# Kernel tuning notes

Hardware: AMD Instinct MI355X
Metric: run time of the kernel (lower is better)

## Reference

```python
import jax, jax.numpy as jnp
import numpy as np

N, D_IN, D_C, D_Q, K = 4096, 64, 32, 128, 3


def setup_inputs() -> dict:
    key = jax.random.key(0)
    ks = jax.random.split(key, 16)
    rn = lambda k, shp, s: jax.random.normal(k, shp, dtype=jnp.float32) * s
    inp = {
        "x": rn(ks[0], (N, D_IN), 1.0),
        "comms": rn(ks[1], (N, D_C), 0.1),
        # dense positive transition matrix (all entries nonzero -> the
        # trans==0 -> -inf masking step is a faithful no-op here)
        "trans": jax.random.uniform(ks[2], (N, N), dtype=jnp.float32, minval=0.01, maxval=1.0),
        "mask": jnp.ones((N,), dtype=jnp.int32),
        # encoding: Linear(num_inputs + comm_channels, ch_q)
        "W_enc": rn(ks[3], (D_IN + D_C, D_Q), 1.0 / np.sqrt(D_IN + D_C)),
        "b_enc": rn(ks[4], (D_Q,), 0.01),
        # att_decoding[k]: Linear(ch_q, ch_q)
        "W_ad": rn(ks[5], (K, D_Q, D_Q), 1.0 / np.sqrt(D_Q)),
        "b_ad": rn(ks[6], (K, D_Q), 0.01),
        # att[k]: Linear(2*ch_q, 1)
        "w_att": rn(ks[7], (K, 2 * D_Q), 1.0 / np.sqrt(2 * D_Q)),
        "b_att": rn(ks[8], (K,), 0.01),
        # att_vectors[k]: Linear(ch_q, ch_q)
        "W_av": rn(ks[9], (K, D_Q, D_Q), 1.0 / np.sqrt(D_Q)),
        "b_av": rn(ks[10], (K, D_Q), 0.01),
        # decoding: Linear(ch_q, 1)
        "W_dec": rn(ks[11], (D_Q,), 1.0 / np.sqrt(D_Q)),
        "b_dec": rn(ks[12], (), 0.01),
    }
    return inp


def reference(x, comms, trans, mask, W_enc, b_enc, W_ad, b_ad, w_att, b_att,
              W_av, b_av, W_dec, b_dec):
    dq = W_ad.shape[-1]
    # encoding of [node features, communication vector]
    h = jnp.concatenate([x, comms], axis=-1) @ W_enc + b_enc          # (n, dq)
    # trans.transpose(0,1); zeros -> -inf (additive log-mask)
    tb = trans.T
    tb = jnp.where(tb == 0, -jnp.inf, tb)                              # (n, n)
    for k in range(K):
        att = h @ W_ad[k] + b_ad[k]                                    # (n, dq)
        # concat-GAT score: score[i,j] = w_a . att[j] + w_b . att[i] + b
        # (decomposition of Linear(cat(att_t, att_t^T)) -> avoids n x n x 2dq)
        wa, wb = w_att[k, :dq], w_att[k, dq:]
        score = (att @ wb)[:, None] + (att @ wa)[None, :] + b_att[k]   # (n, n)
        focus = jax.nn.softmax(score + tb, axis=1)                     # (n, n)
        v = h @ W_av[k] + b_av[k]                                      # (n, dq)
        h = focus @ v                                                  # (n, dq)
    out = h @ W_dec + b_dec                                            # (n,)
    # final masking (args.rl = False branch): masked nodes -> -inf
    s = out + jnp.where(mask == 0, -jnp.inf, 0.0).astype(out.dtype)
    return s
```

## Files before the change

### kernel.cpp

```cpp
#include <hip/hip_runtime.h>
#include <math.h>

#define N 4096
#define DQ 128
#define DIN 64
#define DC 32
#define NT 9
#define PST9 144
#define PST1 16
#define NIT 256

typedef __attribute__((ext_vector_type(8))) short short8;
typedef __attribute__((ext_vector_type(8))) _Float16 half8;
typedef __attribute__((ext_vector_type(4))) float f32x4;

__device__ __forceinline__ unsigned short f2h(float x) {
  return __builtin_bit_cast(unsigned short, (_Float16)x);
}
__device__ __forceinline__ void async16(unsigned short* lds, const unsigned short* g) {
  __builtin_amdgcn_global_load_lds(
      (const __attribute__((address_space(1))) void*)g,
      (__attribute__((address_space(3))) void*)lds, 16, 0, 0);
}

__global__ __launch_bounds__(256) void kExp(const float* __restrict__ trans,
                                            unsigned short* __restrict__ Ef) {
  __shared__ float sh[32 * 65];
  const int tid = threadIdx.x;
  const int ig = blockIdx.x;
  const int kt = blockIdx.y;
  const int r = tid >> 3;
  const int c8 = (tid & 7) * 8;
  const float* src = &trans[((size_t)kt * 32 + r) * N + ig * 64 + c8];
  const float4 v0 = *(const float4*)src;
  const float4 v1 = *(const float4*)(src + 4);
  float* d = &sh[r * 65 + c8];
  d[0] = __expf(v0.x); d[1] = __expf(v0.y); d[2] = __expf(v0.z); d[3] = __expf(v0.w);
  d[4] = __expf(v1.x); d[5] = __expf(v1.y); d[6] = __expf(v1.z); d[7] = __expf(v1.w);
  __syncthreads();
  const int itl = tid >> 6;
  const int lane = tid & 63;
  const int quad = lane >> 4, l15 = lane & 15;
  const int col = itl * 16 + l15;
  unsigned short hb[8];
#pragma unroll
  for (int jj = 0; jj < 8; ++jj) hb[jj] = f2h(sh[(quad * 8 + jj) * 65 + col]);
  const short8 s = {(short)hb[0], (short)hb[1], (short)hb[2], (short)hb[3],
                    (short)hb[4], (short)hb[5], (short)hb[6], (short)hb[7]};
  *(short8*)(Ef + (((size_t)kt * NIT + ig * 4 + itl) * 64 + lane) * 8) = s;
}

__device__ __forceinline__ void v_phase(const float* hs_row, float p,
    const float* __restrict__ W_av_k, const float* __restrict__ b_av_k,
    int r, int d4, unsigned short* shh) {
  float a[4] = {b_av_k[d4], b_av_k[d4 + 1], b_av_k[d4 + 2], b_av_k[d4 + 3]};
  for (int c = 0; c < DQ; ++c) {
    const float hv = hs_row[c];
    const float4 w = *(const float4*)&W_av_k[c * DQ + d4];
    a[0] += hv * w.x; a[1] += hv * w.y; a[2] += hv * w.z; a[3] += hv * w.w;
  }
  const int nt = d4 >> 4;
#pragma unroll
  for (int e = 0; e < 4; ++e)
    shh[nt * 128 + ((d4 + e) & 15) * 8 + r] = f2h(p * a[e]);
  const int c32 = d4 >> 2;
  if (c32 < 16)
    shh[8 * 128 + c32 * 8 + r] = (c32 == 0) ? f2h(p) : 0;
}

__device__ __forceinline__ void v_store(int tid, int blk,
    const unsigned short* shh, unsigned short* __restrict__ Vf) {
  const int kt = blk >> 2, quad = blk & 3;
  if (tid < NT * 16) {
    const int nt = tid >> 4, l15 = tid & 15;
    const size_t dst = (((size_t)kt * NT + nt) * 64 + quad * 16 + l15) * 8;
    *(short8*)(Vf + dst) = *(const short8*)&shh[nt * 128 + l15 * 8];
  }
}

__global__ __launch_bounds__(256) void kVS0(const float* __restrict__ x,
    const float* __restrict__ comms, const float* __restrict__ W_enc,
    const float* __restrict__ b_enc, const float* __restrict__ W_ad_k,
    const float* __restrict__ wa, const float* __restrict__ W_av_k,
    const float* __restrict__ b_av_k, unsigned short* __restrict__ Vf) {
  __shared__ float xs[8][96];
  __shared__ float hs[8][DQ];
  __shared__ float u[DQ];
  __shared__ float pb[8];
  __shared__ __align__(16) unsigned short shh[NT * 128];
  const int tid = threadIdx.x;
  const int blk = blockIdx.x;
  if (tid < 128) {
    const float4 v = *(const float4*)&x[(size_t)blk * 8 * DIN + tid * 4];
    const int idx = tid * 4, r = idx >> 6, c = idx & 63;
    xs[r][c] = v.x; xs[r][c + 1] = v.y; xs[r][c + 2] = v.z; xs[r][c + 3] = v.w;
  } else if (tid < 192) {
    const int t = tid - 128;
    const float4 v = *(const float4*)&comms[(size_t)blk * 8 * DC + t * 4];
    const int idx = t * 4, r = idx >> 5, c = idx & 31;
    xs[r][64 + c] = v.x; xs[r][64 + c + 1] = v.y; xs[r][64 + c + 2] = v.z; xs[r][64 + c + 3] = v.w;
  }
  if (tid < DQ) {
    float s = 0.f;
    const float* wrow = &W_ad_k[tid * DQ];
    for (int q = 0; q < DQ; ++q) s += wrow[q] * wa[q];
    u[tid] = s;
  }
  __syncthreads();
  const int r = tid >> 5;
  const int c32 = tid & 31;
  const int d4 = c32 * 4;
  {
    float a0 = b_enc[d4], a1 = b_enc[d4 + 1], a2 = b_enc[d4 + 2], a3 = b_enc[d4 + 3];
    for (int c = 0; c < 96; ++c) {
      const float hv = xs[r][c];
      const float4 w = *(const float4*)&W_enc[c * DQ + d4];
      a0 += hv * w.x; a1 += hv * w.y; a2 += hv * w.z; a3 += hv * w.w;
    }
    hs[r][d4] = a0; hs[r][d4 + 1] = a1; hs[r][d4 + 2] = a2; hs[r][d4 + 3] = a3;
  }
  __syncthreads();
  float part = 0.f;
  for (int c = c32; c < DQ; c += 32) part += hs[r][c] * u[c];
#pragma unroll
  for (int m = 16; m > 0; m >>= 1) part += __shfl_xor(part, m, 32);
  if (c32 == 0) pb[r] = __expf(part);
  __syncthreads();
  v_phase(hs[r], pb[r], W_av_k, b_av_k, r, d4, shh);
  __syncthreads();
  v_store(tid, blk, shh, Vf);
}

__global__ __launch_bounds__(256) void kVSR(const float* __restrict__ P,
    const float* __restrict__ W_ad_k, const float* __restrict__ wa,
    const float* __restrict__ W_av_k, const float* __restrict__ b_av_k,
    unsigned short* __restrict__ Vf, int ksplit) {
  __shared__ float hs[8][DQ];
  __shared__ float u[DQ];
  __shared__ float pb[8];
  __shared__ __align__(16) unsigned short shh[NT * 128];
  const int tid = threadIdx.x;
  const int r = tid >> 5;
  const int c32 = tid & 31;
  const int d4 = c32 * 4;
  const int j = blockIdx.x * 8 + r;
  if (tid < DQ) {
    float s = 0.f;
    const float* wrow = &W_ad_k[tid * DQ];
    for (int q = 0; q < DQ; ++q) s += wrow[q] * wa[q];
    u[tid] = s;
  }
  float4 num = {0.f, 0.f, 0.f, 0.f};
  float den = 0.f;
  for (int s = 0; s < ksplit; ++s) {
    const float* b = &P[((size_t)s * N + j) * PST9];
    const float4 v = *(const float4*)&b[d4];
    num.x += v.x; num.y += v.y; num.z += v.z; num.w += v.w;
    den += b[128];
  }
  const float inv = 1.f / den;
  hs[r][d4] = num.x * inv; hs[r][d4 + 1] = num.y * inv;
  hs[r][d4 + 2] = num.z * inv; hs[r][d4 + 3] = num.w * inv;
  __syncthreads();
  float part = 0.f;
  for (int c = c32; c < DQ; c += 32) part += hs[r][c] * u[c];
#pragma unroll
  for (int m = 16; m > 0; m >>= 1) part += __shfl_xor(part, m, 32);
  if (c32 == 0) pb[r] = __expf(part);
  __syncthreads();
  v_phase(hs[r], pb[r], W_av_k, b_av_k, r, d4, shh);
  __syncthreads();
  v_store(tid, blockIdx.x, shh, Vf);
}

__global__ __launch_bounds__(256) void kVSRc(const float* __restrict__ P,
    const float* __restrict__ W_ad_k, const float* __restrict__ wa,
    const float* __restrict__ W_av_k, const float* __restrict__ b_av_k,
    const float* __restrict__ W_dec, unsigned short* __restrict__ Vc,
    int ksplit) {
  __shared__ float hs[8][DQ];
  __shared__ float u[DQ];
  __shared__ float pb[8];
  const int tid = threadIdx.x;
  const int r = tid >> 5;
  const int c32 = tid & 31;
  const int d4 = c32 * 4;
  const int j = blockIdx.x * 8 + r;
  if (tid < DQ) {
    float s = 0.f;
    const float* wrow = &W_ad_k[tid * DQ];
    for (int q = 0; q < DQ; ++q) s += wrow[q] * wa[q];
    u[tid] = s;
  }
  float4 num = {0.f, 0.f, 0.f, 0.f};
  float den = 0.f;
  for (int s = 0; s < ksplit; ++s) {
    const float* b = &P[((size_t)s * N + j) * PST9];
    const float4 v = *(const float4*)&b[d4];
    num.x += v.x; num.y += v.y; num.z += v.z; num.w += v.w;
    den += b[128];
  }
  const float inv = 1.f / den;
  hs[r][d4] = num.x * inv; hs[r][d4 + 1] = num.y * inv;
  hs[r][d4 + 2] = num.z * inv; hs[r][d4 + 3] = num.w * inv;
  __syncthreads();
  float part = 0.f;
  for (int c = c32; c < DQ; c += 32) part += hs[r][c] * u[c];
#pragma unroll
  for (int m = 16; m > 0; m >>= 1) part += __shfl_xor(part, m, 32);
  if (c32 == 0) pb[r] = __expf(part);
  __syncthreads();
  float a[4] = {b_av_k[d4], b_av_k[d4 + 1], b_av_k[d4 + 2], b_av_k[d4 + 3]};
  for (int c = 0; c < DQ; ++c) {
    const float hv = hs[r][c];
    const float4 w = *(const float4*)&W_av_k[c * DQ + d4];
    a[0] += hv * w.x; a[1] += hv * w.y; a[2] += hv * w.z; a[3] += hv * w.w;
  }
  float vd = a[0] * W_dec[d4] + a[1] * W_dec[d4 + 1]
           + a[2] * W_dec[d4 + 2] + a[3] * W_dec[d4 + 3];
#pragma unroll
  for (int m = 16; m > 0; m >>= 1) vd += __shfl_xor(vd, m, 32);
  const float p = pb[r];
  if (c32 < 16) {
    const int blk = blockIdx.x;
    const size_t ix = (((size_t)(blk >> 2)) * 64 + (blk & 3) * 16 + c32) * 8 + r;
    Vc[ix] = (c32 == 0) ? f2h(p * vd) : (c32 == 1) ? f2h(p) : 0;
  }
}

template <int NTT, int PST>
__global__ __launch_bounds__(128) void kGemm(
    const unsigned short* __restrict__ Ef, const unsigned short* __restrict__ Vf,
    float* __restrict__ P, int nsteps) {
  __shared__ __align__(16) unsigned short ldsB[2][NTT * 512];
  const int tid = threadIdx.x;
  const int w = tid >> 6, lane = tid & 63;
  const int quad = lane >> 4, l15 = lane & 15;
  const int it0 = blockIdx.x * 4 + w * 2;
  const size_t kt0 = (size_t)blockIdx.y * nsteps;

  for (int c = w; c < NTT; c += 2)
    async16(&ldsB[0][c * 512], Vf + (kt0 * NTT + c) * 512 + lane * 8);
  half8 Ah[2];
#pragma unroll
  for (int ti = 0; ti < 2; ++ti)
    Ah[ti] = __builtin_bit_cast(half8,
        *(const short8*)(Ef + ((kt0 * NIT + it0 + ti) * 64 + lane) * 8));
  f32x4 acc[2][NTT];
#pragma unroll
  for (int ti = 0; ti < 2; ++ti)
#pragma unroll
    for (int nt = 0; nt < NTT; ++nt) acc[ti][nt] = (f32x4){0.f, 0.f, 0.f, 0.f};
  __syncthreads();

  for (int t = 0; t < nsteps; ++t) {
    const bool more = (t + 1 < nsteps);
    half8 nAh[2];
    if (more) {
      const size_t ktn = kt0 + t + 1;
      for (int c = w; c < NTT; c += 2)
        async16(&ldsB[(t + 1) & 1][c * 512], Vf + (ktn * NTT + c) * 512 + lane * 8);
#pragma unroll
      for (int ti = 0; ti < 2; ++ti)
        nAh[ti] = __builtin_bit_cast(half8,
            *(const short8*)(Ef + ((ktn * NIT + it0 + ti) * 64 + lane) * 8));
    }
    const unsigned short* bb = ldsB[t & 1];
#pragma unroll
    for (int nt = 0; nt < NTT; ++nt) {
      const half8 Bh = __builtin_bit_cast(half8, *(const short8*)(bb + nt * 512 + lane * 8));
      acc[0][nt] = __builtin_amdgcn_mfma_f32_16x16x32_f16(Ah[0], Bh, acc[0][nt], 0, 0, 0);
      acc[1][nt] = __builtin_amdgcn_mfma_f32_16x16x32_f16(Ah[1], Bh, acc[1][nt], 0, 0, 0);
    }
    if (more) {
      Ah[0] = nAh[0]; Ah[1] = nAh[1];
      __syncthreads();
    }
  }
  float* Pb = P + (size_t)blockIdx.y * N * PST;
#pragma unroll
  for (int ti = 0; ti < 2; ++ti) {
#pragma unroll
    for (int nt = 0; nt < NTT; ++nt) {
#pragma unroll
      for (int r = 0; r < 4; ++r) {
        const int i = (it0 + ti) * 16 + quad * 4 + r;
        Pb[(size_t)i * PST + nt * 16 + l15] = acc[ti][nt][r];
      }
    }
  }
}

__global__ __launch_bounds__(256) void kOut(const float* __restrict__ P3,
    const float* __restrict__ b_dec, const int* __restrict__ mask,
    float* __restrict__ out, int ksplit) {
  const int i = blockIdx.x * 256 + threadIdx.x;
  float num = 0.f, den = 0.f;
  for (int s = 0; s < ksplit; ++s) {
    const float* b = &P3[((size_t)s * N + i) * PST1];
    num += b[0];
    den += b[1];
  }
  out[i] = (mask[i] == 0) ? -INFINITY : num / den + b_dec[0];
}

extern "C" void kernel_launch(void* const* d_in, const int* in_sizes, int n_in,
                              void* d_out, int out_size, void* d_ws, size_t ws_size,
                              hipStream_t stream) {
  (void)in_sizes; (void)n_in; (void)out_size;
  const float* x     = (const float*)d_in[0];
  const float* comms = (const float*)d_in[1];
  const float* trans = (const float*)d_in[2];
  const int*   mask  = (const int*)d_in[3];
  const float* W_enc = (const float*)d_in[4];
  const float* b_enc = (const float*)d_in[5];
  const float* W_ad  = (const float*)d_in[6];
  const float* w_att = (const float*)d_in[8];
  const float* W_av  = (const float*)d_in[10];
  const float* b_av  = (const float*)d_in[11];
  const float* W_dec = (const float*)d_in[12];
  const float* b_dec = (const float*)d_in[13];
  float* out         = (float*)d_out;

  char* ws = (char*)d_ws;
  unsigned short* Vf = (unsigned short*)ws;  ws += (size_t)(N / 32) * NT * 512 * 2;
  unsigned short* Vc = (unsigned short*)ws;  ws += (size_t)(N / 32) * 512 * 2;
  unsigned short* Ef = (unsigned short*)ws;  ws += (size_t)N * N * 2;
  float* P  = (float*)ws;
  const size_t fixedB = (size_t)(N / 32) * (NT + 1) * 1024 + (size_t)N * N * 2;
  const size_t perB   = (size_t)N * (PST9 + PST1) * 4;
  const int ksplit = (ws_size >= fixedB + 16 * perB) ? 16 : 8;
  float* P3 = P + (size_t)ksplit * N * PST9;
  const int nsteps = (N / ksplit) >> 5;

  kExp<<<dim3(64, 128), 256, 0, stream>>>(trans, Ef);
  const float* wa1 = w_att;
  kVS0<<<N / 8, 256, 0, stream>>>(x, comms, W_enc, b_enc, W_ad, wa1,
                                  W_av, b_av, Vf);
  kGemm<NT, PST9><<<dim3(NIT / 4, ksplit), 128, 0, stream>>>(Ef, Vf, P, nsteps);

  kVSR<<<N / 8, 256, 0, stream>>>(P, W_ad + (size_t)1 * DQ * DQ,
                                  w_att + 2 * DQ, W_av + (size_t)1 * DQ * DQ,
                                  b_av + DQ, Vf, ksplit);
  kGemm<NT, PST9><<<dim3(NIT / 4, ksplit), 128, 0, stream>>>(Ef, Vf, P, nsteps);

  kVSRc<<<N / 8, 256, 0, stream>>>(P, W_ad + (size_t)2 * DQ * DQ,
                                   w_att + 4 * DQ, W_av + (size_t)2 * DQ * DQ,
                                   b_av + 2 * DQ, W_dec, Vc, ksplit);
  kGemm<1, PST1><<<dim3(NIT / 4, ksplit), 128, 0, stream>>>(Ef, Vc, P3, nsteps);

  kOut<<<N / 256, 256, 0, stream>>>(P3, b_dec, mask, out, ksplit);
}
```

Measured before the change: 227.5 us.

## Batch eight k-steps per stage and widen GEMM blocks to four waves

The split-K GEMM kernel now uses 256-thread blocks of four waves, so each block covers 8 row tiles instead of 4. Instead of double-buffering one k-step at a time, it loads 8 k-steps of B into LDS and 8 A fragments into registers, then runs all their MFMAs between barriers. This cuts barrier count and lets more loads be in flight at once, and B reuse per block doubles. In exchange there is no overlap between a stage's loads and its compute, register pressure rises from the 16 A fragments, and LDS per block grows to 8*NT*1KB (72KB for NT=9), which may limit occupancy.

Result: no change. 229.5 us (+0.9%).

```diff
diff --git a/kernel.cpp b/kernel.cpp
--- a/kernel.cpp
+++ b/kernel.cpp
@@ -229,52 +229,43 @@
 }
 
 template <int NTT, int PST>
-__global__ __launch_bounds__(128) void kGemm(
+__global__ __launch_bounds__(256) void kGemm(
     const unsigned short* __restrict__ Ef, const unsigned short* __restrict__ Vf,
     float* __restrict__ P, int nsteps) {
-  __shared__ __align__(16) unsigned short ldsB[2][NTT * 512];
+  __shared__ __align__(16) unsigned short lds[8 * NTT * 512];
   const int tid = threadIdx.x;
   const int w = tid >> 6, lane = tid & 63;
   const int quad = lane >> 4, l15 = lane & 15;
-  const int it0 = blockIdx.x * 4 + w * 2;
-  const size_t kt0 = (size_t)blockIdx.y * nsteps;
-
-  for (int c = w; c < NTT; c += 2)
-    async16(&ldsB[0][c * 512], Vf + (kt0 * NTT + c) * 512 + lane * 8);
-  half8 Ah[2];
+  const int it0 = blockIdx.x * 8 + w * 2;
+
+  f32x4 acc[2][NTT];
 #pragma unroll
   for (int ti = 0; ti < 2; ++ti)
-    Ah[ti] = __builtin_bit_cast(half8,
-        *(const short8*)(Ef + ((kt0 * NIT + it0 + ti) * 64 + lane) * 8));
-  f32x4 acc[2][NTT];
-#pragma unroll
-  for (int ti = 0; ti < 2; ++ti)
 #pragma unroll
     for (int nt = 0; nt < NTT; ++nt) acc[ti][nt] = (f32x4){0.f, 0.f, 0.f, 0.f};
-  __syncthreads();
-
-  for (int t = 0; t < nsteps; ++t) {
-    const bool more = (t + 1 < nsteps);
-    half8 nAh[2];
-    if (more) {
-      const size_t ktn = kt0 + t + 1;
-      for (int c = w; c < NTT; c += 2)
-        async16(&ldsB[(t + 1) & 1][c * 512], Vf + (ktn * NTT + c) * 512 + lane * 8);
-#pragma unroll
-      for (int ti = 0; ti < 2; ++ti)
-        nAh[ti] = __builtin_bit_cast(half8,
-            *(const short8*)(Ef + ((ktn * NIT + it0 + ti) * 64 + lane) * 8));
-    }
-    const unsigned short* bb = ldsB[t & 1];
-#pragma unroll
-    for (int nt = 0; nt < NTT; ++nt) {
-      const half8 Bh = __builtin_bit_cast(half8, *(const short8*)(bb + nt * 512 + lane * 8));
-      acc[0][nt] = __builtin_amdgcn_mfma_f32_16x16x32_f16(Ah[0], Bh, acc[0][nt], 0, 0, 0);
-      acc[1][nt] = __builtin_amdgcn_mfma_f32_16x16x32_f16(Ah[1], Bh, acc[1][nt], 0, 0, 0);
-    }
-    if (more) {
-      Ah[0] = nAh[0]; Ah[1] = nAh[1];
-      __syncthreads();
+
+  for (int ss = 0; ss < nsteps; ss += 8) {
+    const size_t kt0 = (size_t)blockIdx.y * nsteps + ss;
+    if (ss) __syncthreads();
+    for (int c = w; c < 8 * NTT; c += 4)
+      async16(&lds[c * 512], Vf + (kt0 * NTT + c) * 512 + lane * 8);
+    half8 A[2][8];
+#pragma unroll
+    for (int ti = 0; ti < 2; ++ti)
+#pragma unroll
+      for (int s = 0; s < 8; ++s)
+        A[ti][s] = __builtin_bit_cast(half8,
+            *(const short8*)(Ef + (((kt0 + s) * NIT + it0 + ti) * 64 + lane) * 8));
+    __syncthreads();
+#pragma unroll
+    for (int s = 0; s < 8; ++s) {
+#pragma unroll
+      for (int nt = 0; nt < NTT; ++nt) {
+        const half8 Bh = __builtin_bit_cast(half8,
+            *(const short8*)(lds + (s * NTT + nt) * 512 + lane * 8));
+        acc[0][nt] = __builtin_amdgcn_mfma_f32_16x16x32_f16(A[0][s], Bh, acc[0][nt], 0, 0, 0);
+        acc[1][nt] = __builtin_amdgcn_mfma_f32_16x16x32_f16(A[1][s], Bh, acc[1][nt], 0, 0, 0);
+      }
     }
   }
   float* Pb = P + (size_t)blockIdx.y * N * PST;
@@ -334,20 +325,19 @@
   const int nsteps = (N / ksplit) >> 5;
 
   kExp<<<dim3(64, 128), 256, 0, stream>>>(trans, Ef);
-  const float* wa1 = w_att;
-  kVS0<<<N / 8, 256, 0, stream>>>(x, comms, W_enc, b_enc, W_ad, wa1,
+  kVS0<<<N / 8, 256, 0, stream>>>(x, comms, W_enc, b_enc, W_ad, w_att,
                                   W_av, b_av, Vf);
-  kGemm<NT, PST9><<<dim3(NIT / 4, ksplit), 128, 0, stream>>>(Ef, Vf, P, nsteps);
+  kGemm<NT, PST9><<<dim3(NIT / 8, ksplit), 256, 0, stream>>>(Ef, Vf, P, nsteps);
 
   kVSR<<<N / 8, 256, 0, stream>>>(P, W_ad + (size_t)1 * DQ * DQ,
                                   w_att + 2 * DQ, W_av + (size_t)1 * DQ * DQ,
                                   b_av + DQ, Vf, ksplit);
-  kGemm<NT, PST9><<<dim3(NIT / 4, ksplit), 128, 0, stream>>>(Ef, Vf, P, nsteps);
+  kGemm<NT, PST9><<<dim3(NIT / 8, ksplit), 256, 0, stream>>>(Ef, Vf, P, nsteps);
 
   kVSRc<<<N / 8, 256, 0, stream>>>(P, W_ad + (size_t)2 * DQ * DQ,
                                    w_att + 4 * DQ, W_av + (size_t)2 * DQ * DQ,
                                    b_av + 2 * DQ, W_dec, Vc, ksplit);
-  kGemm<1, PST1><<<dim3(NIT / 4, ksplit), 128, 0, stream>>>(Ef, Vc, P3, nsteps);
+  kGemm<1, PST1><<<dim3(NIT / 8, ksplit), 256, 0, stream>>>(Ef, Vc, P3, nsteps);
 
   kOut<<<N / 256, 256, 0, stream>>>(P3, b_dec, mask, out, ksplit);
 }
```
